# Kernel tuning notes

Hardware: AMD Instinct MI355X
Metric: run time of the kernel (lower is better)

Reference implementation:

```python
import jax, jax.numpy as jnp
import numpy as np

B = 4          # num_batches
R = 128        # resolution per axis (cubic grid)
N = 4_194_304  # total sample points
EMA_DECAY = 0.95


def setup_inputs() -> dict:
    key = jax.random.key(0)
    k1, k2, k3, k4 = jax.random.split(key, 4)
    occ_val_grid = jax.random.uniform(k1, (B, R, R, R), dtype=jnp.float32)
    pts = jax.random.uniform(k2, (N, 3), minval=-1.0, maxval=1.0, dtype=jnp.float32)
    occ_val = jax.random.uniform(k3, (N,), dtype=jnp.float32)
    bidx = jax.random.randint(k4, (N,), 0, B, dtype=jnp.int32)
    return dict(occ_val_grid=occ_val_grid, pts=pts, occ_val=occ_val, bidx=bidx)


def reference(occ_val_grid, pts, occ_val, bidx):
    """Faithful port of update_batched_occ_val_grid_ (bidx path):
    1) quantize normalized pts in [-1,1] to integer voxel coords, clamped;
    2) ravel (bidx, gx, gy, gz) -> flat index;
    3) scatter_max of occ_val into an EMA-decayed copy of the grid;
    4) write back only at the touched indices (index_put_), so untouched
       voxels keep their OLD, non-decayed value."""
    res = jnp.array([R, R, R], dtype=jnp.int32)
    # ((pts/2 + 0.5) * res).long().clamp(0, res-1)
    gidx = ((pts / 2.0 + 0.5) * res.astype(pts.dtype)).astype(jnp.int32)
    gidx = jnp.clip(gidx, 0, res - 1)                      # [N, 3]
    strides = jnp.array([R * R, R, 1], dtype=jnp.int32)
    idx_ravel = bidx * (R * R * R) + (gidx * strides).sum(-1)  # [N]

    flat = occ_val_grid.reshape(-1)                        # [B*R^3]
    decayed = EMA_DECAY * flat                             # scatter_max 'out' buffer
    occ_val_new = decayed.at[idx_ravel].max(occ_val)       # scatter_max with out=decayed
    # index_put_ writeback: only touched voxels get the new (decayed/maxed) value
    out = flat.at[idx_ravel].set(occ_val_new[idx_ravel])
    return out.reshape(B, R, R, R)
```

## Files before the change

### kernel.cpp

```cpp
#include <hip/hip_runtime.h>
#include <hip/hip_bf16.h>


#define GRID_R          128
#define EMA_DEC         0.95f
#define NBUCKET         512
#define VOX_PER_BUCKET  16384
#define PTS_PER_BLOCK   16384
#define K1_THREADS      1024
#define PTS_PER_THREAD  16

__device__ __forceinline__ int quant_clamp(float p) {
    int g = (int)((p * 0.5f + 0.5f) * (float)GRID_R);
    return min(max(g, 0), GRID_R - 1);
}

__global__ __launch_bounds__(1024)
void occ_localsort4_kernel(const float* __restrict__ pts,
                           const float* __restrict__ occ_val,
                           const int*   __restrict__ bidx,
                           unsigned*        __restrict__ sorted,
                           unsigned short*  __restrict__ offT,
                           int n_total, int nchunk) {
    extern __shared__ unsigned rec[];
    __shared__ int cur[NBUCKET];
    __shared__ int wsum[8];

    const int tid  = threadIdx.x;
    const int lane = tid & 63;
    const int wv   = tid >> 6;
    const int c    = blockIdx.x;

    for (int b = tid; b < NBUCKET; b += K1_THREADS) cur[b] = 0;
    __syncthreads();

    const float4* pts4 = reinterpret_cast<const float4*>(pts);
    const float4* ov4  = reinterpret_cast<const float4*>(occ_val);
    const int4*   bi4  = reinterpret_cast<const int4*>(bidx);

    int pk[PTS_PER_THREAD];
    int bk[PTS_PER_THREAD];

    #pragma unroll
    for (int r = 0; r < PTS_PER_THREAD / 8; ++r) {
        const int i = c * ((PTS_PER_THREAD / 8) * K1_THREADS)
                    + r * K1_THREADS + tid;
        if (i * 8 + 7 < n_total) {
            float4 q0 = pts4[i * 6 + 0];
            float4 q1 = pts4[i * 6 + 1];
            float4 q2 = pts4[i * 6 + 2];
            float4 q3 = pts4[i * 6 + 3];
            float4 q4 = pts4[i * 6 + 4];
            float4 q5 = pts4[i * 6 + 5];
            float4 oa = ov4[i * 2 + 0];
            float4 ob = ov4[i * 2 + 1];
            int4   ba = bi4[i * 2 + 0];
            int4   bb = bi4[i * 2 + 1];

            float xs[8] = {q0.x, q0.w, q1.z, q2.y, q3.x, q3.w, q4.z, q5.y};
            float ys[8] = {q0.y, q1.x, q1.w, q2.z, q3.y, q4.x, q4.w, q5.z};
            float zs[8] = {q0.z, q1.y, q2.x, q2.w, q3.z, q4.y, q5.x, q5.w};
            int   vb[8] = {__float_as_int(oa.x), __float_as_int(oa.y),
                           __float_as_int(oa.z), __float_as_int(oa.w),
                           __float_as_int(ob.x), __float_as_int(ob.y),
                           __float_as_int(ob.z), __float_as_int(ob.w)};
            int   bs[8] = {ba.x, ba.y, ba.z, ba.w, bb.x, bb.y, bb.z, bb.w};

            #pragma unroll
            for (int k = 0; k < 8; ++k) {
                int gx = quant_clamp(xs[k]);
                int gy = quant_clamp(ys[k]);
                int gz = quant_clamp(zs[k]);
                int idx = bs[k] * (GRID_R * GRID_R * GRID_R)
                        + gx * (GRID_R * GRID_R) + gy * GRID_R + gz;
                pk[r * 8 + k] = (vb[k] & (int)0xFFFFC000) | (idx & 0x3FFF);
                bk[r * 8 + k] = idx >> 14;
            }
        } else {
            #pragma unroll
            for (int k = 0; k < 8; ++k) {
                bk[r * 8 + k] = -1;
                pk[r * 8 + k] = 0;
                int p = i * 8 + k;
                if (p < n_total) {
                    int gx = quant_clamp(pts[p * 3 + 0]);
                    int gy = quant_clamp(pts[p * 3 + 1]);
                    int gz = quant_clamp(pts[p * 3 + 2]);
                    int idx = bidx[p] * (GRID_R * GRID_R * GRID_R)
                            + gx * (GRID_R * GRID_R) + gy * GRID_R + gz;
                    pk[r * 8 + k] = (__float_as_int(occ_val[p]) & (int)0xFFFFC000)
                                  | (idx & 0x3FFF);
                    bk[r * 8 + k] = idx >> 14;
                }
            }
        }
    }

    #pragma unroll
    for (int k = 0; k < PTS_PER_THREAD; ++k)
        if (bk[k] >= 0) atomicAdd(&cur[bk[k]], 1);
    __syncthreads();

    int a = 0, x = 0;
    if (tid < NBUCKET) {
        a = cur[tid];
        x = a;
        #pragma unroll
        for (int off = 1; off < 64; off <<= 1) {
            int v = __shfl_up(x, off, 64);
            if (lane >= off) x += v;
        }
        if (lane == 63) wsum[wv] = x;
    }
    __syncthreads();

    int total_sh;
    if (tid < NBUCKET) {
        int wofs = 0;
        #pragma unroll
        for (int w = 0; w < 8; ++w) if (w < wv) wofs += wsum[w];
        const int excl = x + wofs - a;
        offT[(size_t)tid * nchunk + c] = (unsigned short)excl;
        cur[tid] = excl;
        if (tid == 0) {
            int total = wsum[0] + wsum[1] + wsum[2] + wsum[3]
                      + wsum[4] + wsum[5] + wsum[6] + wsum[7];
            offT[(size_t)NBUCKET * nchunk + c] = (unsigned short)total;
        }
    }
    __syncthreads();

    #pragma unroll
    for (int k = 0; k < PTS_PER_THREAD; ++k) {
        if (bk[k] >= 0) {
            int slot = atomicAdd(&cur[bk[k]], 1);
            rec[slot] = (unsigned)pk[k];
        }
    }
    __syncthreads();

    total_sh = cur[NBUCKET - 1];
    unsigned* dst = sorted + (size_t)c * PTS_PER_BLOCK;
    for (int j = tid; j < total_sh; j += K1_THREADS)
        dst[j] = rec[j];
}

__global__ __launch_bounds__(1024)
void occ_bucket7_kernel(const unsigned*       __restrict__ sorted,
                        const unsigned short* __restrict__ offT,
                        const float*          __restrict__ grid,
                        float*                __restrict__ out,
                        int nchunk) {
    __shared__ int smax[VOX_PER_BUCKET];
    const int tid = threadIdx.x;
    const int b = (blockIdx.x & 7) * (NBUCKET / 8) + (blockIdx.x >> 3);

    int4* s4 = reinterpret_cast<int4*>(smax);
    for (int j = tid; j < VOX_PER_BUCKET / 4; j += 1024)
        s4[j] = make_int4(-1, -1, -1, -1);
    __syncthreads();

    const unsigned short* rowLo = offT + (size_t)b       * nchunk;
    const unsigned short* rowHi = offT + (size_t)(b + 1) * nchunk;

    for (int t = tid; t < nchunk * 4; t += 1024) {
        const int c  = t >> 2;
        const int p  = t & 3;
        const int lo = rowLo[c];
        const int hi = rowHi[c];
        const unsigned* rp = sorted + (size_t)c * PTS_PER_BLOCK;
        for (int j = (lo & ~3) + 4 * p; j < hi; j += 16) {
            uint4 e = *reinterpret_cast<const uint4*>(rp + j);
            if (j     >= lo && j     < hi)
                atomicMax(&smax[e.x & (VOX_PER_BUCKET - 1)], (int)e.x);
            if (j + 1 >= lo && j + 1 < hi)
                atomicMax(&smax[e.y & (VOX_PER_BUCKET - 1)], (int)e.y);
            if (j + 2 >= lo && j + 2 < hi)
                atomicMax(&smax[e.z & (VOX_PER_BUCKET - 1)], (int)e.z);
            if (j + 3 >= lo && j + 3 < hi)
                atomicMax(&smax[e.w & (VOX_PER_BUCKET - 1)], (int)e.w);
        }
    }
    __syncthreads();

    const size_t vbase = (size_t)b * VOX_PER_BUCKET;
    const float4* g4  = reinterpret_cast<const float4*>(grid + vbase);
    float4*       o4  = reinterpret_cast<float4*>(out + vbase);
    const int4*   sm4 = reinterpret_cast<const int4*>(smax);
    for (int j = tid; j < VOX_PER_BUCKET / 4; j += 1024) {
        int4   w = sm4[j];
        float4 g = g4[j];
        float4 r;
        r.x = (w.x == -1) ? g.x
            : fmaxf(EMA_DEC * g.x, __int_as_float(w.x & (int)0xFFFFC000));
        r.y = (w.y == -1) ? g.y
            : fmaxf(EMA_DEC * g.y, __int_as_float(w.y & (int)0xFFFFC000));
        r.z = (w.z == -1) ? g.z
            : fmaxf(EMA_DEC * g.z, __int_as_float(w.z & (int)0xFFFFC000));
        r.w = (w.w == -1) ? g.w
            : fmaxf(EMA_DEC * g.w, __int_as_float(w.w & (int)0xFFFFC000));
        o4[j] = r;
    }
}

__global__ void occ_scatter8_kernel(const float* __restrict__ pts,
                                    const float* __restrict__ occ_val,
                                    const int*   __restrict__ bidx,
                                    int*         __restrict__ out_bits,
                                    int n8, int n_total) {
    const int tid    = blockIdx.x * blockDim.x + threadIdx.x;
    const int stride = gridDim.x * blockDim.x;

    const float4* pts4 = reinterpret_cast<const float4*>(pts);
    const float4* ov4  = reinterpret_cast<const float4*>(occ_val);
    const int4*   bi4  = reinterpret_cast<const int4*>(bidx);

    for (int i = tid; i < n8; i += stride) {
        float4 q0 = pts4[i * 6 + 0];
        float4 q1 = pts4[i * 6 + 1];
        float4 q2 = pts4[i * 6 + 2];
        float4 q3 = pts4[i * 6 + 3];
        float4 q4 = pts4[i * 6 + 4];
        float4 q5 = pts4[i * 6 + 5];
        float4 oa = ov4[i * 2 + 0];
        float4 ob = ov4[i * 2 + 1];
        int4   ba = bi4[i * 2 + 0];
        int4   bb = bi4[i * 2 + 1];

        float xs[8] = {q0.x, q0.w, q1.z, q2.y, q3.x, q3.w, q4.z, q5.y};
        float ys[8] = {q0.y, q1.x, q1.w, q2.z, q3.y, q4.x, q4.w, q5.z};
        float zs[8] = {q0.z, q1.y, q2.x, q2.w, q3.z, q4.y, q5.x, q5.w};
        int   vb[8] = {__float_as_int(oa.x), __float_as_int(oa.y),
                       __float_as_int(oa.z), __float_as_int(oa.w),
                       __float_as_int(ob.x), __float_as_int(ob.y),
                       __float_as_int(ob.z), __float_as_int(ob.w)};
        int   bs[8] = {ba.x, ba.y, ba.z, ba.w, bb.x, bb.y, bb.z, bb.w};

        int idx[8];
        #pragma unroll
        for (int k = 0; k < 8; ++k) {
            int gx = quant_clamp(xs[k]);
            int gy = quant_clamp(ys[k]);
            int gz = quant_clamp(zs[k]);
            idx[k] = bs[k] * (GRID_R * GRID_R * GRID_R)
                   + gx * (GRID_R * GRID_R) + gy * GRID_R + gz;
        }
        #pragma unroll
        for (int k = 0; k < 8; ++k) atomicMax(&out_bits[idx[k]], vb[k]);
    }

    for (int i = n8 * 8 + tid; i < n_total; i += stride) {
        int gx = quant_clamp(pts[i * 3 + 0]);
        int gy = quant_clamp(pts[i * 3 + 1]);
        int gz = quant_clamp(pts[i * 3 + 2]);
        int idx = bidx[i] * (GRID_R * GRID_R * GRID_R)
                + gx * (GRID_R * GRID_R) + gy * GRID_R + gz;
        atomicMax(&out_bits[idx], __float_as_int(occ_val[i]));
    }
}

__global__ void occ_finalize_kernel(const float* __restrict__ grid,
                                    float*       __restrict__ out,
                                    int v4, int v_total) {
    const int tid    = blockIdx.x * blockDim.x + threadIdx.x;
    const int stride = gridDim.x * blockDim.x;

    const float4* g4 = reinterpret_cast<const float4*>(grid);
    int4*         w4 = reinterpret_cast<int4*>(out);
    float4*       o4 = reinterpret_cast<float4*>(out);

    for (int i = tid; i < v4; i += stride) {
        int4   w = w4[i];
        float4 g = g4[i];
        float4 r;
        r.x = (w.x == -1) ? g.x : fmaxf(EMA_DEC * g.x, __int_as_float(w.x));
        r.y = (w.y == -1) ? g.y : fmaxf(EMA_DEC * g.y, __int_as_float(w.y));
        r.z = (w.z == -1) ? g.z : fmaxf(EMA_DEC * g.z, __int_as_float(w.z));
        r.w = (w.w == -1) ? g.w : fmaxf(EMA_DEC * g.w, __int_as_float(w.w));
        o4[i] = r;
    }
    for (int i = v4 * 4 + tid; i < v_total; i += stride) {
        int w = reinterpret_cast<int*>(out)[i];
        float g = grid[i];
        out[i] = (w == -1) ? g : fmaxf(EMA_DEC * g, __int_as_float(w));
    }
}

extern "C" void kernel_launch(void* const* d_in, const int* in_sizes, int n_in,
                              void* d_out, int out_size, void* d_ws, size_t ws_size,
                              hipStream_t stream) {
    const float* grid    = (const float*)d_in[0];
    const float* pts     = (const float*)d_in[1];
    const float* occ_val = (const float*)d_in[2];
    const int*   bidx    = (const int*)d_in[3];

    float* out = (float*)d_out;
    const int N = in_sizes[2];

    const int nchunk = (N + PTS_PER_BLOCK - 1) / PTS_PER_BLOCK;

    const size_t sorted_b = (size_t)nchunk * PTS_PER_BLOCK * sizeof(unsigned);
    const size_t off_b    = (size_t)(NBUCKET + 1) * nchunk * sizeof(unsigned short);
    const size_t need     = sorted_b + off_b + 16;
    const bool shape_ok   = (out_size == 4 * GRID_R * GRID_R * GRID_R);

    if (ws_size >= need && shape_ok && nchunk >= 1 && nchunk < 65536) {
        unsigned*       sorted = (unsigned*)d_ws;
        unsigned short* offT   = (unsigned short*)((char*)d_ws + sorted_b);

        occ_localsort4_kernel<<<nchunk, K1_THREADS,
                                PTS_PER_BLOCK * sizeof(unsigned), stream>>>(
            pts, occ_val, bidx, sorted, offT, N, nchunk);
        occ_bucket7_kernel<<<NBUCKET, 1024, 0, stream>>>(
            sorted, offT, grid, out, nchunk);
    } else {
        hipMemsetAsync(d_out, 0xFF, (size_t)out_size * sizeof(float), stream);

        const int n8 = N / 8;
        int sblocks = (n8 + 255) / 256;
        if (sblocks < 1) sblocks = 1;
        occ_scatter8_kernel<<<sblocks, 256, 0, stream>>>(
            pts, occ_val, bidx, (int*)d_out, n8, N);

        const int v4 = out_size / 4;
        int fblocks = (v4 + 255) / 256;
        if (fblocks > 2048) fblocks = 2048;
        if (fblocks < 1) fblocks = 1;
        occ_finalize_kernel<<<fblocks, 256, 0, stream>>>(grid, out, v4, out_size);
    }
}
```

Baseline: 37.58 us.

## Pad per-bucket segments to multiples of four and halve sort chunk size

```diff
diff --git a/kernel.cpp b/kernel.cpp
--- a/kernel.cpp
+++ b/kernel.cpp
@@ -6,17 +6,18 @@
 #define EMA_DEC         0.95f
 #define NBUCKET         512
 #define VOX_PER_BUCKET  16384
-#define PTS_PER_BLOCK   16384
-#define K1_THREADS      1024
+#define PTS_PER_BLOCK   8192
+#define K1_THREADS      512
 #define PTS_PER_THREAD  16
+#define REC_CAP         (PTS_PER_BLOCK + NBUCKET * 3)
 
 __device__ __forceinline__ int quant_clamp(float p) {
     int g = (int)((p * 0.5f + 0.5f) * (float)GRID_R);
     return min(max(g, 0), GRID_R - 1);
 }
 
-__global__ __launch_bounds__(1024)
-void occ_localsort4_kernel(const float* __restrict__ pts,
+__global__ __launch_bounds__(512)
+void occ_localsort5_kernel(const float* __restrict__ pts,
                            const float* __restrict__ occ_val,
                            const int*   __restrict__ bidx,
                            unsigned*        __restrict__ sorted,
@@ -25,6 +26,7 @@
     extern __shared__ unsigned rec[];
     __shared__ int cur[NBUCKET];
     __shared__ int wsum[8];
+    __shared__ int sh_total;
 
     const int tid  = threadIdx.x;
     const int lane = tid & 63;
@@ -32,6 +34,7 @@
     const int c    = blockIdx.x;
 
     for (int b = tid; b < NBUCKET; b += K1_THREADS) cur[b] = 0;
+    for (int j = tid; j < REC_CAP; j += K1_THREADS) rec[j] = 0xFFFFFFFFu;
     __syncthreads();
 
     const float4* pts4 = reinterpret_cast<const float4*>(pts);
@@ -101,31 +104,27 @@
         if (bk[k] >= 0) atomicAdd(&cur[bk[k]], 1);
     __syncthreads();
 
-    int a = 0, x = 0;
-    if (tid < NBUCKET) {
-        a = cur[tid];
-        x = a;
-        #pragma unroll
-        for (int off = 1; off < 64; off <<= 1) {
-            int v = __shfl_up(x, off, 64);
-            if (lane >= off) x += v;
-        }
-        if (lane == 63) wsum[wv] = x;
-    }
-    __syncthreads();
-
-    int total_sh;
-    if (tid < NBUCKET) {
+    const int a  = cur[tid];
+    const int ra = (a + 3) & ~3;
+    int x = ra;
+    #pragma unroll
+    for (int off = 1; off < 64; off <<= 1) {
+        int v = __shfl_up(x, off, 64);
+        if (lane >= off) x += v;
+    }
+    if (lane == 63) wsum[wv] = x;
+    __syncthreads();
+
+    {
         int wofs = 0;
         #pragma unroll
         for (int w = 0; w < 8; ++w) if (w < wv) wofs += wsum[w];
-        const int excl = x + wofs - a;
+        const int excl = x + wofs - ra;
         offT[(size_t)tid * nchunk + c] = (unsigned short)excl;
         cur[tid] = excl;
-        if (tid == 0) {
-            int total = wsum[0] + wsum[1] + wsum[2] + wsum[3]
-                      + wsum[4] + wsum[5] + wsum[6] + wsum[7];
-            offT[(size_t)NBUCKET * nchunk + c] = (unsigned short)total;
+        if (tid == K1_THREADS - 1) {
+            sh_total = excl + ra;
+            offT[(size_t)NBUCKET * nchunk + c] = (unsigned short)(excl + ra);
         }
     }
     __syncthreads();
@@ -139,14 +138,14 @@
     }
     __syncthreads();
 
-    total_sh = cur[NBUCKET - 1];
-    unsigned* dst = sorted + (size_t)c * PTS_PER_BLOCK;
-    for (int j = tid; j < total_sh; j += K1_THREADS)
+    const int total = sh_total;
+    unsigned* dst = sorted + (size_t)c * REC_CAP;
+    for (int j = tid; j < total; j += K1_THREADS)
         dst[j] = rec[j];
 }
 
 __global__ __launch_bounds__(1024)
-void occ_bucket7_kernel(const unsigned*       __restrict__ sorted,
+void occ_bucket8_kernel(const unsigned*       __restrict__ sorted,
                         const unsigned short* __restrict__ offT,
                         const float*          __restrict__ grid,
                         float*                __restrict__ out,
@@ -168,17 +167,13 @@
         const int p  = t & 3;
         const int lo = rowLo[c];
         const int hi = rowHi[c];
-        const unsigned* rp = sorted + (size_t)c * PTS_PER_BLOCK;
-        for (int j = (lo & ~3) + 4 * p; j < hi; j += 16) {
+        const unsigned* rp = sorted + (size_t)c * REC_CAP;
+        for (int j = lo + 4 * p; j < hi; j += 16) {
             uint4 e = *reinterpret_cast<const uint4*>(rp + j);
-            if (j     >= lo && j     < hi)
-                atomicMax(&smax[e.x & (VOX_PER_BUCKET - 1)], (int)e.x);
-            if (j + 1 >= lo && j + 1 < hi)
-                atomicMax(&smax[e.y & (VOX_PER_BUCKET - 1)], (int)e.y);
-            if (j + 2 >= lo && j + 2 < hi)
-                atomicMax(&smax[e.z & (VOX_PER_BUCKET - 1)], (int)e.z);
-            if (j + 3 >= lo && j + 3 < hi)
-                atomicMax(&smax[e.w & (VOX_PER_BUCKET - 1)], (int)e.w);
+            atomicMax(&smax[e.x & (VOX_PER_BUCKET - 1)], (int)e.x);
+            atomicMax(&smax[e.y & (VOX_PER_BUCKET - 1)], (int)e.y);
+            atomicMax(&smax[e.z & (VOX_PER_BUCKET - 1)], (int)e.z);
+            atomicMax(&smax[e.w & (VOX_PER_BUCKET - 1)], (int)e.w);
         }
     }
     __syncthreads();
@@ -299,7 +294,7 @@
 
     const int nchunk = (N + PTS_PER_BLOCK - 1) / PTS_PER_BLOCK;
 
-    const size_t sorted_b = (size_t)nchunk * PTS_PER_BLOCK * sizeof(unsigned);
+    const size_t sorted_b = (size_t)nchunk * REC_CAP * sizeof(unsigned);
     const size_t off_b    = (size_t)(NBUCKET + 1) * nchunk * sizeof(unsigned short);
     const size_t need     = sorted_b + off_b + 16;
     const bool shape_ok   = (out_size == 4 * GRID_R * GRID_R * GRID_R);
@@ -308,10 +303,10 @@
         unsigned*       sorted = (unsigned*)d_ws;
         unsigned short* offT   = (unsigned short*)((char*)d_ws + sorted_b);
 
-        occ_localsort4_kernel<<<nchunk, K1_THREADS,
-                                PTS_PER_BLOCK * sizeof(unsigned), stream>>>(
+        occ_localsort5_kernel<<<nchunk, K1_THREADS,
+                                REC_CAP * sizeof(unsigned), stream>>>(
             pts, occ_val, bidx, sorted, offT, N, nchunk);
-        occ_bucket7_kernel<<<NBUCKET, 1024, 0, stream>>>(
+        occ_bucket8_kernel<<<NBUCKET, 1024, 0, stream>>>(
             sorted, offT, grid, out, nchunk);
     } else {
         hipMemsetAsync(d_out, 0xFF, (size_t)out_size * sizeof(float), stream);
```

Result: no change. 37.94 us (+1.0%).
